# Performance work log

Measured on AMD Instinct MI355X. Metric: run time of the kernel, lower is better.

The kernel has to match this reference:

```python
import jax, jax.numpy as jnp
import numpy as np

N_NODES = 100000


def _gcn_layer(h, W, b, src, dst, norm, n):
    # h: [N, Fin] -> transform then normalized scatter-add aggregation
    h = h @ W                                   # [N, Fout]
    msg = h[src] * norm[:, None]                # [E', Fout] gather + scale
    out = jax.ops.segment_sum(msg, dst, num_segments=n)  # scatter-add
    return out + b


def setup_inputs() -> dict:
    key = jax.random.key(0)
    k1, k2, k3, k4 = jax.random.split(key, 4)
    N, F_IN, HID, C, E = N_NODES, 512, 128, 40, 1600000
    x = jax.random.normal(k1, (N, F_IN), dtype=jnp.float32)
    edge_index = jax.random.randint(k2, (2, E), 0, N, dtype=jnp.int64)
    W1 = jax.random.normal(k3, (F_IN, HID), dtype=jnp.float32) * (1.0 / np.sqrt(F_IN))
    b1 = jnp.zeros((HID,), dtype=jnp.float32)
    W2 = jax.random.normal(k4, (HID, C), dtype=jnp.float32) * (1.0 / np.sqrt(HID))
    b2 = jnp.zeros((C,), dtype=jnp.float32)
    return {"x": x, "edge_index": edge_index, "W1": W1, "b1": b1, "W2": W2, "b2": b2}


def reference(x, edge_index, W1, b1, W2, b2):
    n = x.shape[0]
    # add self-loops (GCNConv default)
    loop = jnp.arange(n, dtype=edge_index.dtype)
    src = jnp.concatenate([edge_index[0], loop])
    dst = jnp.concatenate([edge_index[1], loop])
    # symmetric normalization: deg counted on destination (in-degree, incl. self-loop)
    deg = jax.ops.segment_sum(jnp.ones_like(dst, dtype=x.dtype), dst, num_segments=n)
    dis = jnp.where(deg > 0, jax.lax.rsqrt(deg), 0.0)  # deg^{-1/2}
    norm = dis[src] * dis[dst]                          # per-edge weight

    h = jax.nn.relu(_gcn_layer(x, W1, b1, src, dst, norm, n))
    # dropout: identity in eval mode (training=False)
    h = _gcn_layer(h, W2, b2, src, dst, norm, n)
    return jax.nn.log_softmax(h, axis=1)
```

## Files before the change

### kernel.cpp

```cpp
#include <hip/hip_runtime.h>
#include <hip/hip_bf16.h>


#define F_IN 512
#define HID  128
#define NC   40

typedef __attribute__((ext_vector_type(8))) short bf16x8;
typedef __attribute__((ext_vector_type(4))) float f32x4v;

__device__ __forceinline__ ushort f2bf(float f) {
    union { float f; unsigned u; } x; x.f = f;
    unsigned r = x.u + 0x7FFFu + ((x.u >> 16) & 1u);
    return (ushort)(r >> 16);
}
__device__ __forceinline__ float bf2f(ushort u) {
    return __uint_as_float((unsigned)u << 16);
}
__device__ __forceinline__ bf16x8 cvt8(float4 lo, float4 hi) {
    __align__(16) ushort t[8];
    t[0]=f2bf(lo.x); t[1]=f2bf(lo.y); t[2]=f2bf(lo.z); t[3]=f2bf(lo.w);
    t[4]=f2bf(hi.x); t[5]=f2bf(hi.y); t[6]=f2bf(hi.z); t[7]=f2bf(hi.w);
    return *(const bf16x8*)t;
}

__global__ void prep_k(const int* __restrict__ dst, int E, int EB,
                       unsigned* __restrict__ cnt,
                       const float* __restrict__ W1, const float* __restrict__ W2,
                       ushort* __restrict__ W1p, ushort* __restrict__ W2p) {
    int b = blockIdx.x;
    if (b < EB) {
        int t = b * 256 + threadIdx.x;
        if (t < E) atomicAdd(&cnt[dst[t]], 1u);
        return;
    }
    int t = (b - EB) * 256 + threadIdx.x;
    if (t < 65536) {
        int j = t & 7, n = (t >> 3) & 127, kb = (t >> 10) & 3, s = t >> 12;
        int k = s * 32 + kb * 8 + j;
        W1p[t] = f2bf(W1[(size_t)k * HID + n]);
    } else {
        int q = t - 65536;
        if (q < 6144) {
            int j = q & 7;
            int i2 = q >> 3;
            int n = i2 % 48;
            int i3 = i2 / 48;
            int kb = i3 & 3, ks = i3 >> 2;
            int k = ks * 32 + kb * 8 + j;
            float v = (n < NC) ? W2[(size_t)k * NC + n] : 0.f;
            W2p[q] = f2bf(v);
        }
    }
}

__global__ __launch_bounds__(1024) void scan_block(const unsigned* __restrict__ cnt,
                                                   unsigned* __restrict__ offs,
                                                   unsigned* __restrict__ bsums,
                                                   float* __restrict__ dis, int N) {
    int tid = threadIdx.x;
    int i = blockIdx.x * 1024 + tid;
    unsigned v = (i < N) ? cnt[i] : 0u;
    if (i < N) dis[i] = rsqrtf((float)v + 1.0f);
    int lane = tid & 63, w = tid >> 6;
    unsigned s = v;
    #pragma unroll
    for (int d = 1; d < 64; d <<= 1) {
        unsigned t = __shfl_up(s, d, 64);
        if (lane >= d) s += t;
    }
    __shared__ unsigned wt[16];
    if (lane == 63) wt[w] = s;
    __syncthreads();
    unsigned add = 0;
    #pragma unroll
    for (int j = 0; j < 16; j++) add += (j < w) ? wt[j] : 0u;
    unsigned incl = s + add;
    if (i < N) offs[i] = incl - v;
    if (tid == 1023) bsums[blockIdx.x] = incl;
}

__global__ __launch_bounds__(1024) void scan_add2(unsigned* __restrict__ offs,
                                                  const unsigned* __restrict__ bsums,
                                                  int N, unsigned total) {
    int i = blockIdx.x * 1024 + threadIdx.x;
    int lane = threadIdx.x & 63;
    unsigned s = 0;
    for (int j = lane; j < (int)blockIdx.x; j += 64) s += bsums[j];
    #pragma unroll
    for (int d = 1; d < 64; d <<= 1) s += __shfl_xor(s, d, 64);
    if (i < N) offs[i] += s;
    if (i == 0) offs[N] = total;
}

__global__ void fill_csr(const int* __restrict__ src, const int* __restrict__ dst,
                         const unsigned* __restrict__ offs, unsigned* __restrict__ cursor,
                         int* __restrict__ col, int E) {
    int t = blockIdx.x * blockDim.x + threadIdx.x;
    if (t >= E) return;
    int s = src[t], d = dst[t];
    unsigned pos = offs[d] + atomicAdd(&cursor[d], 1u);
    col[pos] = s;
}

__global__ __launch_bounds__(256) void gemm1_mfma(const float* __restrict__ A,
                                                  const ushort* __restrict__ Bp,
                                                  const float* __restrict__ dis,
                                                  ushort* __restrict__ C, int N) {
    const int tid  = threadIdx.x;
    const int wave = tid >> 6;
    const int lane = tid & 63;
    const int quad = lane >> 4;
    const int mr   = lane & 15;
    const int base = (blockIdx.x * 4 + wave) * 32;
    if (base >= N) return;
    const int r0 = base + mr;
    const int r1 = base + 16 + mr;
    const bool ok0 = r0 < N, ok1 = r1 < N;
    const float* ap0 = A + (size_t)(ok0 ? r0 : 0) * F_IN + quad * 8;
    const float* ap1 = A + (size_t)(ok1 ? r1 : 0) * F_IN + quad * 8;
    const ushort* bp = Bp + quad * 1024 + mr * 8;

    f32x4v acc0[8], acc1[8];
    #pragma unroll
    for (int t = 0; t < 8; t++) {
        acc0[t] = (f32x4v){0.f, 0.f, 0.f, 0.f};
        acc1[t] = (f32x4v){0.f, 0.f, 0.f, 0.f};
    }

    float4 av[2][4];
    #pragma unroll
    for (int b = 0; b < 2; b++) {
        av[b][0] = *(const float4*)(ap0 + b * 32);
        av[b][1] = *(const float4*)(ap0 + b * 32 + 4);
        av[b][2] = *(const float4*)(ap1 + b * 32);
        av[b][3] = *(const float4*)(ap1 + b * 32 + 4);
    }

    for (int s = 0; s < 16; s++) {
        bf16x8 fa0 = cvt8(av[s & 1][0], av[s & 1][1]);
        bf16x8 fa1 = cvt8(av[s & 1][2], av[s & 1][3]);
        if (s < 14) {
            av[s & 1][0] = *(const float4*)(ap0 + (s + 2) * 32);
            av[s & 1][1] = *(const float4*)(ap0 + (s + 2) * 32 + 4);
            av[s & 1][2] = *(const float4*)(ap1 + (s + 2) * 32);
            av[s & 1][3] = *(const float4*)(ap1 + (s + 2) * 32 + 4);
        }
        const ushort* bs = bp + s * 4096;
        #pragma unroll
        for (int t = 0; t < 8; t++) {
            bf16x8 b = *(const bf16x8*)(bs + t * 128);
            acc0[t] = __builtin_amdgcn_mfma_f32_16x16x32_bf16(fa0, b, acc0[t], 0, 0, 0);
            acc1[t] = __builtin_amdgcn_mfma_f32_16x16x32_bf16(fa1, b, acc1[t], 0, 0, 0);
        }
    }

    #pragma unroll
    for (int rr = 0; rr < 4; rr++) {
        int ra = base + quad * 4 + rr;
        if (ra < N) {
            float ds = dis[ra];
            #pragma unroll
            for (int t = 0; t < 8; t++)
                C[(size_t)ra * HID + t * 16 + mr] = f2bf(acc0[t][rr] * ds);
        }
        int rb = base + 16 + quad * 4 + rr;
        if (rb < N) {
            float ds = dis[rb];
            #pragma unroll
            for (int t = 0; t < 8; t++)
                C[(size_t)rb * HID + t * 16 + mr] = f2bf(acc1[t][rr] * ds);
        }
    }
}

__global__ __launch_bounds__(256) void agg1_k(const ushort* __restrict__ h,
                                              const int* __restrict__ col,
                                              const unsigned* __restrict__ offs,
                                              const float* __restrict__ dis,
                                              const float* __restrict__ b1,
                                              ushort* __restrict__ out, int N) {
    int node = blockIdx.x * 16 + (threadIdx.x >> 4);
    if (node >= N) return;
    int lane = threadIdx.x & 15;
    const ushort* hb = h + (size_t)lane * 8;
    float a[8];
    {
        uint4 v = *(const uint4*)(hb + (size_t)node * HID);
        const ushort* u = (const ushort*)&v;
        #pragma unroll
        for (int j = 0; j < 8; j++) a[j] = bf2f(u[j]);
    }
    unsigned p0 = offs[node], p1 = offs[node + 1];
    unsigned p = p0;
    while (p < p1 && (p & 3u)) {
        int s = col[p++];
        uint4 v = *(const uint4*)(hb + (size_t)s * HID);
        const ushort* u = (const ushort*)&v;
        #pragma unroll
        for (int j = 0; j < 8; j++) a[j] += bf2f(u[j]);
    }
    unsigned rem = p1 - p;
    const int4* cp = (const int4*)(col + p);
    unsigned nb8 = rem >> 3;
    int4 c0, c1;
    if (nb8) { c0 = cp[0]; c1 = cp[1]; }
    for (unsigned b = 0; b < nb8; b++) {
        uint4 v0 = *(const uint4*)(hb + (size_t)c0.x * HID);
        uint4 v1 = *(const uint4*)(hb + (size_t)c0.y * HID);
        uint4 v2 = *(const uint4*)(hb + (size_t)c0.z * HID);
        uint4 v3 = *(const uint4*)(hb + (size_t)c0.w * HID);
        uint4 v4 = *(const uint4*)(hb + (size_t)c1.x * HID);
        uint4 v5 = *(const uint4*)(hb + (size_t)c1.y * HID);
        uint4 v6 = *(const uint4*)(hb + (size_t)c1.z * HID);
        uint4 v7 = *(const uint4*)(hb + (size_t)c1.w * HID);
        if (b + 1 < nb8) { c0 = cp[2 * b + 2]; c1 = cp[2 * b + 3]; }
        const ushort* u0 = (const ushort*)&v0;
        const ushort* u1 = (const ushort*)&v1;
        const ushort* u2 = (const ushort*)&v2;
        const ushort* u3 = (const ushort*)&v3;
        const ushort* u4 = (const ushort*)&v4;
        const ushort* u5 = (const ushort*)&v5;
        const ushort* u6 = (const ushort*)&v6;
        const ushort* u7 = (const ushort*)&v7;
        #pragma unroll
        for (int j = 0; j < 8; j++) {
            float t0 = bf2f(u0[j]) + bf2f(u1[j]);
            float t1 = bf2f(u2[j]) + bf2f(u3[j]);
            float t2 = bf2f(u4[j]) + bf2f(u5[j]);
            float t3 = bf2f(u6[j]) + bf2f(u7[j]);
            a[j] += (t0 + t1) + (t2 + t3);
        }
    }
    p += nb8 << 3;
    if (rem & 4u) {
        int4 c = *(const int4*)(col + p);
        uint4 v0 = *(const uint4*)(hb + (size_t)c.x * HID);
        uint4 v1 = *(const uint4*)(hb + (size_t)c.y * HID);
        uint4 v2 = *(const uint4*)(hb + (size_t)c.z * HID);
        uint4 v3 = *(const uint4*)(hb + (size_t)c.w * HID);
        const ushort* u0 = (const ushort*)&v0;
        const ushort* u1 = (const ushort*)&v1;
        const ushort* u2 = (const ushort*)&v2;
        const ushort* u3 = (const ushort*)&v3;
        #pragma unroll
        for (int j = 0; j < 8; j++)
            a[j] += (bf2f(u0[j]) + bf2f(u1[j])) + (bf2f(u2[j]) + bf2f(u3[j]));
        p += 4;
    }
    for (; p < p1; ++p) {
        int s = col[p];
        uint4 v = *(const uint4*)(hb + (size_t)s * HID);
        const ushort* u = (const ushort*)&v;
        #pragma unroll
        for (int j = 0; j < 8; j++) a[j] += bf2f(u[j]);
    }
    float dd = dis[node];
    float4 bb0 = *(const float4*)(b1 + lane * 8);
    float4 bb1 = *(const float4*)(b1 + lane * 8 + 4);
    const float bb[8] = {bb0.x, bb0.y, bb0.z, bb0.w, bb1.x, bb1.y, bb1.z, bb1.w};
    __align__(16) ushort o[8];
    #pragma unroll
    for (int j = 0; j < 8; j++) o[j] = f2bf(fmaxf(a[j] * dd + bb[j], 0.f));
    *(uint4*)(out + (size_t)node * HID + (size_t)lane * 8) = *(const uint4*)o;
}

__global__ __launch_bounds__(256) void gemm2_mfma(const ushort* __restrict__ A,
                                                  const ushort* __restrict__ W2p,
                                                  const float* __restrict__ dis,
                                                  ushort* __restrict__ h2, int N) {
    const int tid  = threadIdx.x;
    const int wave = tid >> 6;
    const int lane = tid & 63;
    const int quad = lane >> 4;
    const int mr   = lane & 15;
    const int base = (blockIdx.x * 4 + wave) * 32;
    if (base >= N) return;
    const int r0 = base + mr;
    const int r1 = base + 16 + mr;
    const bool ok0 = r0 < N, ok1 = r1 < N;
    const ushort* ap0 = A + (size_t)(ok0 ? r0 : 0) * HID + quad * 8;
    const ushort* ap1 = A + (size_t)(ok1 ? r1 : 0) * HID + quad * 8;
    const ushort* bp = W2p + quad * 384 + mr * 8;

    f32x4v acc0[3], acc1[3];
    #pragma unroll
    for (int t = 0; t < 3; t++) {
        acc0[t] = (f32x4v){0.f, 0.f, 0.f, 0.f};
        acc1[t] = (f32x4v){0.f, 0.f, 0.f, 0.f};
    }
    #pragma unroll
    for (int ks = 0; ks < 4; ks++) {
        bf16x8 a0 = *(const bf16x8*)(ap0 + ks * 32);
        bf16x8 a1 = *(const bf16x8*)(ap1 + ks * 32);
        #pragma unroll
        for (int t = 0; t < 3; t++) {
            bf16x8 b = *(const bf16x8*)(bp + ks * 1536 + t * 128);
            acc0[t] = __builtin_amdgcn_mfma_f32_16x16x32_bf16(a0, b, acc0[t], 0, 0, 0);
            acc1[t] = __builtin_amdgcn_mfma_f32_16x16x32_bf16(a1, b, acc1[t], 0, 0, 0);
        }
    }
    #pragma unroll
    for (int rr = 0; rr < 4; rr++) {
        int ra = base + quad * 4 + rr;
        if (ra < N) {
            float ds = dis[ra];
            #pragma unroll
            for (int t = 0; t < 3; t++) {
                int c = t * 16 + mr;
                if (c < NC) h2[(size_t)ra * NC + c] = f2bf(acc0[t][rr] * ds);
            }
        }
        int rb = base + 16 + quad * 4 + rr;
        if (rb < N) {
            float ds = dis[rb];
            #pragma unroll
            for (int t = 0; t < 3; t++) {
                int c = t * 16 + mr;
                if (c < NC) h2[(size_t)rb * NC + c] = f2bf(acc1[t][rr] * ds);
            }
        }
    }
}

__global__ __launch_bounds__(256) void agg2_ls(const ushort* __restrict__ h2,
                                               const int* __restrict__ col,
                                               const unsigned* __restrict__ offs,
                                               const float* __restrict__ dis,
                                               const float* __restrict__ b2,
                                               float* __restrict__ out, int N) {
    int node = blockIdx.x * 32 + (threadIdx.x >> 3);
    if (node >= N) return;
    int lane = threadIdx.x & 7;
    const bool act = lane < 5;
    const ushort* hb = h2 + (size_t)lane * 8;
    float a[8] = {};
    if (act) {
        uint4 v = *(const uint4*)(hb + (size_t)node * NC);
        const ushort* u = (const ushort*)&v;
        #pragma unroll
        for (int j = 0; j < 8; j++) a[j] = bf2f(u[j]);
    }
    unsigned p0 = offs[node], p1 = offs[node + 1];
    unsigned p = p0;
    while (p < p1 && (p & 3u)) {
        int s = col[p++];
        if (act) {
            uint4 v = *(const uint4*)(hb + (size_t)s * NC);
            const ushort* u = (const ushort*)&v;
            #pragma unroll
            for (int j = 0; j < 8; j++) a[j] += bf2f(u[j]);
        }
    }
    unsigned rem = p1 - p;
    const int4* cp = (const int4*)(col + p);
    unsigned nb8 = rem >> 3;
    int4 c0, c1;
    if (nb8) { c0 = cp[0]; c1 = cp[1]; }
    for (unsigned b = 0; b < nb8; b++) {
        int s0 = c0.x, s1 = c0.y, s2 = c0.z, s3 = c0.w;
        int s4 = c1.x, s5 = c1.y, s6 = c1.z, s7 = c1.w;
        if (b + 1 < nb8) { c0 = cp[2 * b + 2]; c1 = cp[2 * b + 3]; }
        if (act) {
            uint4 v0 = *(const uint4*)(hb + (size_t)s0 * NC);
            uint4 v1 = *(const uint4*)(hb + (size_t)s1 * NC);
            uint4 v2 = *(const uint4*)(hb + (size_t)s2 * NC);
            uint4 v3 = *(const uint4*)(hb + (size_t)s3 * NC);
            uint4 v4 = *(const uint4*)(hb + (size_t)s4 * NC);
            uint4 v5 = *(const uint4*)(hb + (size_t)s5 * NC);
            uint4 v6 = *(const uint4*)(hb + (size_t)s6 * NC);
            uint4 v7 = *(const uint4*)(hb + (size_t)s7 * NC);
            const ushort* u0 = (const ushort*)&v0;
            const ushort* u1 = (const ushort*)&v1;
            const ushort* u2 = (const ushort*)&v2;
            const ushort* u3 = (const ushort*)&v3;
            const ushort* u4 = (const ushort*)&v4;
            const ushort* u5 = (const ushort*)&v5;
            const ushort* u6 = (const ushort*)&v6;
            const ushort* u7 = (const ushort*)&v7;
            #pragma unroll
            for (int j = 0; j < 8; j++) {
                float t0 = bf2f(u0[j]) + bf2f(u1[j]);
                float t1 = bf2f(u2[j]) + bf2f(u3[j]);
                float t2 = bf2f(u4[j]) + bf2f(u5[j]);
                float t3 = bf2f(u6[j]) + bf2f(u7[j]);
                a[j] += (t0 + t1) + (t2 + t3);
            }
        }
    }
    p += nb8 << 3;
    if (rem & 4u) {
        int4 c = *(const int4*)(col + p);
        if (act) {
            uint4 v0 = *(const uint4*)(hb + (size_t)c.x * NC);
            uint4 v1 = *(const uint4*)(hb + (size_t)c.y * NC);
            uint4 v2 = *(const uint4*)(hb + (size_t)c.z * NC);
            uint4 v3 = *(const uint4*)(hb + (size_t)c.w * NC);
            const ushort* u0 = (const ushort*)&v0;
            const ushort* u1 = (const ushort*)&v1;
            const ushort* u2 = (const ushort*)&v2;
            const ushort* u3 = (const ushort*)&v3;
            #pragma unroll
            for (int j = 0; j < 8; j++)
                a[j] += (bf2f(u0[j]) + bf2f(u1[j])) + (bf2f(u2[j]) + bf2f(u3[j]));
        }
        p += 4;
    }
    for (; p < p1; ++p) {
        int s = col[p];
        if (act) {
            uint4 v = *(const uint4*)(hb + (size_t)s * NC);
            const ushort* u = (const ushort*)&v;
            #pragma unroll
            for (int j = 0; j < 8; j++) a[j] += bf2f(u[j]);
        }
    }
    float dd = dis[node];
    float l[8];
    float m = -1e30f;
    if (act) {
        #pragma unroll
        for (int j = 0; j < 8; j++) {
            l[j] = a[j] * dd + b2[lane * 8 + j];
            m = fmaxf(m, l[j]);
        }
    }
    #pragma unroll
    for (int d = 1; d < 8; d <<= 1) m = fmaxf(m, __shfl_xor(m, d, 8));
    float s = 0.f;
    if (act) {
        #pragma unroll
        for (int j = 0; j < 8; j++) s += __expf(l[j] - m);
    }
    #pragma unroll
    for (int d = 1; d < 8; d <<= 1) s += __shfl_xor(s, d, 8);
    float lse = m + __logf(s);
    if (act) {
        float* op = out + (size_t)node * NC + lane * 8;
        *(float4*)op       = make_float4(l[0]-lse, l[1]-lse, l[2]-lse, l[3]-lse);
        *(float4*)(op + 4) = make_float4(l[4]-lse, l[5]-lse, l[6]-lse, l[7]-lse);
    }
}

extern "C" void kernel_launch(void* const* d_in, const int* in_sizes, int n_in,
                              void* d_out, int out_size, void* d_ws, size_t ws_size,
                              hipStream_t stream) {
    const float* x  = (const float*)d_in[0];
    const int*   ei = (const int*)d_in[1];
    const float* W1 = (const float*)d_in[2];
    const float* b1 = (const float*)d_in[3];
    const float* W2 = (const float*)d_in[4];
    const float* b2 = (const float*)d_in[5];
    float* out = (float*)d_out;

    const int N = in_sizes[0] / F_IN;
    const int E = in_sizes[1] / 2;
    const int* src = ei;
    const int* dst = ei + E;

    char* ws = (char*)d_ws;
    size_t o = 0;
    unsigned* cnt  = (unsigned*)(ws + o); o += (size_t)N * 4;
    unsigned* cur  = (unsigned*)(ws + o); o += (size_t)N * 4;
    float*    dis  = (float*)   (ws + o); o += (size_t)N * 4;
    unsigned* offs = (unsigned*)(ws + o); o += (size_t)(N + 4) * 4;
    unsigned* bsums= (unsigned*)(ws + o); o += 4096;
    int*      col  = (int*)     (ws + o); o += (size_t)E * 4;
    o = (o + 15) & ~(size_t)15;
    ushort*   W1p  = (ushort*)  (ws + o); o += (size_t)F_IN * HID * 2;
    o = (o + 15) & ~(size_t)15;
    ushort*   W2p  = (ushort*)  (ws + o); o += 6144 * 2;
    o = (o + 15) & ~(size_t)15;
    ushort*   h1   = (ushort*)  (ws + o); o += (size_t)N * HID * 2;
    o = (o + 15) & ~(size_t)15;
    ushort*   ag1  = (ushort*)  (ws + o); o += (size_t)N * HID * 2;
    o = (o + 15) & ~(size_t)15;
    ushort*   h2   = (ushort*)  (ws + o); o += (size_t)N * NC * 2;

    const int nb = (N + 1023) / 1024;
    const int EB = (E + 255) / 256;
    const int PB = (65536 + 6144 + 255) / 256;

    hipMemsetAsync(cnt, 0, (size_t)N * 8, stream);
    prep_k<<<EB + PB, 256, 0, stream>>>(dst, E, EB, cnt, W1, W2, W1p, W2p);
    scan_block<<<nb, 1024, 0, stream>>>(cnt, offs, bsums, dis, N);
    scan_add2<<<nb, 1024, 0, stream>>>(offs, bsums, N, (unsigned)E);
    fill_csr<<<(E + 255) / 256, 256, 0, stream>>>(src, dst, offs, cur, col, E);

    gemm1_mfma<<<(N + 127) / 128, 256, 0, stream>>>(x, W1p, dis, h1, N);
    agg1_k<<<(N + 15) / 16, 256, 0, stream>>>(h1, col, offs, dis, b1, ag1, N);

    gemm2_mfma<<<(N + 127) / 128, 256, 0, stream>>>(ag1, W2p, dis, h2, N);
    agg2_ls<<<(N + 31) / 32, 256, 0, stream>>>(h2, col, offs, dis, b2, out, N);
}
```

Before: 597.4 us.

## Fuse CSR fill into GEMM1, widen aggregation to full waves, pad h2, use hardware bf16 pack

Merges the CSR fill kernel and the first GEMM into one launch, with the two kinds of blocks doing independent work. Both aggregation kernels now give each node a full 64-lane wave that splits its neighbour list across sub-groups and combines them with shuffle reductions. This aims to raise memory-level parallelism on the gathers at the cost of idle lanes for low-degree nodes. It also pads the second-layer features to 48 columns so rows are 16-byte aligned, and replaces software bf16 rounding with the v_cvt_pk_bf16_f32 instruction.

```diff
diff --git a/kernel.cpp b/kernel.cpp
--- a/kernel.cpp
+++ b/kernel.cpp
@@ -5,23 +5,29 @@
 #define F_IN 512
 #define HID  128
 #define NC   40
+#define NCP  48
 
 typedef __attribute__((ext_vector_type(8))) short bf16x8;
 typedef __attribute__((ext_vector_type(4))) float f32x4v;
 
 __device__ __forceinline__ ushort f2bf(float f) {
-    union { float f; unsigned u; } x; x.f = f;
-    unsigned r = x.u + 0x7FFFu + ((x.u >> 16) & 1u);
-    return (ushort)(r >> 16);
+    unsigned r;
+    asm("v_cvt_pk_bf16_f32 %0, %1, %1" : "=v"(r) : "v"(f));
+    return (ushort)r;
+}
+__device__ __forceinline__ unsigned cvtpk(float a, float b) {
+    unsigned r;
+    asm("v_cvt_pk_bf16_f32 %0, %1, %2" : "=v"(r) : "v"(a), "v"(b));
+    return r;
 }
 __device__ __forceinline__ float bf2f(ushort u) {
     return __uint_as_float((unsigned)u << 16);
 }
 __device__ __forceinline__ bf16x8 cvt8(float4 lo, float4 hi) {
-    __align__(16) ushort t[8];
-    t[0]=f2bf(lo.x); t[1]=f2bf(lo.y); t[2]=f2bf(lo.z); t[3]=f2bf(lo.w);
-    t[4]=f2bf(hi.x); t[5]=f2bf(hi.y); t[6]=f2bf(hi.z); t[7]=f2bf(hi.w);
-    return *(const bf16x8*)t;
+    union { unsigned u[4]; bf16x8 v; } t;
+    t.u[0] = cvtpk(lo.x, lo.y); t.u[1] = cvtpk(lo.z, lo.w);
+    t.u[2] = cvtpk(hi.x, hi.y); t.u[3] = cvtpk(hi.z, hi.w);
+    return t.v;
 }
 
 __global__ void prep_k(const int* __restrict__ dst, int E, int EB,
@@ -93,20 +99,21 @@
     if (i == 0) offs[N] = total;
 }
 
-__global__ void fill_csr(const int* __restrict__ src, const int* __restrict__ dst,
-                         const unsigned* __restrict__ offs, unsigned* __restrict__ cursor,
-                         int* __restrict__ col, int E) {
-    int t = blockIdx.x * blockDim.x + threadIdx.x;
-    if (t >= E) return;
-    int s = src[t], d = dst[t];
-    unsigned pos = offs[d] + atomicAdd(&cursor[d], 1u);
-    col[pos] = s;
-}
-
-__global__ __launch_bounds__(256) void gemm1_mfma(const float* __restrict__ A,
-                                                  const ushort* __restrict__ Bp,
-                                                  const float* __restrict__ dis,
-                                                  ushort* __restrict__ C, int N) {
+__global__ __launch_bounds__(256) void fill_gemm1(
+        const int* __restrict__ src, const int* __restrict__ dst,
+        const unsigned* __restrict__ offs, unsigned* __restrict__ cursor,
+        int* __restrict__ col, int E, int GB,
+        const float* __restrict__ A, const ushort* __restrict__ Bp,
+        const float* __restrict__ dis, ushort* __restrict__ C, int N) {
+    if (blockIdx.x >= GB) {
+        int t = (blockIdx.x - GB) * 256 + threadIdx.x;
+        if (t < E) {
+            int s = src[t], d = dst[t];
+            unsigned pos = offs[d] + atomicAdd(&cursor[d], 1u);
+            col[pos] = s;
+        }
+        return;
+    }
     const int tid  = threadIdx.x;
     const int wave = tid >> 6;
     const int lane = tid & 63;
@@ -180,89 +187,54 @@
                                               const float* __restrict__ dis,
                                               const float* __restrict__ b1,
                                               ushort* __restrict__ out, int N) {
-    int node = blockIdx.x * 16 + (threadIdx.x >> 4);
+    int node = blockIdx.x * 4 + (threadIdx.x >> 6);
     if (node >= N) return;
-    int lane = threadIdx.x & 15;
-    const ushort* hb = h + (size_t)lane * 8;
-    float a[8];
-    {
+    int lane = threadIdx.x & 63;
+    int ni = lane >> 4;
+    int fl = lane & 15;
+    const ushort* hb = h + (size_t)fl * 8;
+    float a[8] = {0.f, 0.f, 0.f, 0.f, 0.f, 0.f, 0.f, 0.f};
+    if (ni == 0) {
         uint4 v = *(const uint4*)(hb + (size_t)node * HID);
         const ushort* u = (const ushort*)&v;
         #pragma unroll
         for (int j = 0; j < 8; j++) a[j] = bf2f(u[j]);
     }
     unsigned p0 = offs[node], p1 = offs[node + 1];
-    unsigned p = p0;
-    while (p < p1 && (p & 3u)) {
-        int s = col[p++];
-        uint4 v = *(const uint4*)(hb + (size_t)s * HID);
-        const ushort* u = (const ushort*)&v;
-        #pragma unroll
-        for (int j = 0; j < 8; j++) a[j] += bf2f(u[j]);
-    }
-    unsigned rem = p1 - p;
-    const int4* cp = (const int4*)(col + p);
-    unsigned nb8 = rem >> 3;
-    int4 c0, c1;
-    if (nb8) { c0 = cp[0]; c1 = cp[1]; }
-    for (unsigned b = 0; b < nb8; b++) {
-        uint4 v0 = *(const uint4*)(hb + (size_t)c0.x * HID);
-        uint4 v1 = *(const uint4*)(hb + (size_t)c0.y * HID);
-        uint4 v2 = *(const uint4*)(hb + (size_t)c0.z * HID);
-        uint4 v3 = *(const uint4*)(hb + (size_t)c0.w * HID);
-        uint4 v4 = *(const uint4*)(hb + (size_t)c1.x * HID);
-        uint4 v5 = *(const uint4*)(hb + (size_t)c1.y * HID);
-        uint4 v6 = *(const uint4*)(hb + (size_t)c1.z * HID);
-        uint4 v7 = *(const uint4*)(hb + (size_t)c1.w * HID);
-        if (b + 1 < nb8) { c0 = cp[2 * b + 2]; c1 = cp[2 * b + 3]; }
-        const ushort* u0 = (const ushort*)&v0;
-        const ushort* u1 = (const ushort*)&v1;
-        const ushort* u2 = (const ushort*)&v2;
-        const ushort* u3 = (const ushort*)&v3;
-        const ushort* u4 = (const ushort*)&v4;
-        const ushort* u5 = (const ushort*)&v5;
-        const ushort* u6 = (const ushort*)&v6;
-        const ushort* u7 = (const ushort*)&v7;
-        #pragma unroll
-        for (int j = 0; j < 8; j++) {
-            float t0 = bf2f(u0[j]) + bf2f(u1[j]);
-            float t1 = bf2f(u2[j]) + bf2f(u3[j]);
-            float t2 = bf2f(u4[j]) + bf2f(u5[j]);
-            float t3 = bf2f(u6[j]) + bf2f(u7[j]);
-            a[j] += (t0 + t1) + (t2 + t3);
-        }
-    }
-    p += nb8 << 3;
-    if (rem & 4u) {
-        int4 c = *(const int4*)(col + p);
-        uint4 v0 = *(const uint4*)(hb + (size_t)c.x * HID);
-        uint4 v1 = *(const uint4*)(hb + (size_t)c.y * HID);
-        uint4 v2 = *(const uint4*)(hb + (size_t)c.z * HID);
-        uint4 v3 = *(const uint4*)(hb + (size_t)c.w * HID);
-        const ushort* u0 = (const ushort*)&v0;
-        const ushort* u1 = (const ushort*)&v1;
-        const ushort* u2 = (const ushort*)&v2;
-        const ushort* u3 = (const ushort*)&v3;
-        #pragma unroll
-        for (int j = 0; j < 8; j++)
-            a[j] += (bf2f(u0[j]) + bf2f(u1[j])) + (bf2f(u2[j]) + bf2f(u3[j]));
-        p += 4;
-    }
-    for (; p < p1; ++p) {
-        int s = col[p];
-        uint4 v = *(const uint4*)(hb + (size_t)s * HID);
-        const ushort* u = (const ushort*)&v;
-        #pragma unroll
-        for (int j = 0; j < 8; j++) a[j] += bf2f(u[j]);
-    }
-    float dd = dis[node];
-    float4 bb0 = *(const float4*)(b1 + lane * 8);
-    float4 bb1 = *(const float4*)(b1 + lane * 8 + 4);
-    const float bb[8] = {bb0.x, bb0.y, bb0.z, bb0.w, bb1.x, bb1.y, bb1.z, bb1.w};
-    __align__(16) ushort o[8];
-    #pragma unroll
-    for (int j = 0; j < 8; j++) o[j] = f2bf(fmaxf(a[j] * dd + bb[j], 0.f));
-    *(uint4*)(out + (size_t)node * HID + (size_t)lane * 8) = *(const uint4*)o;
+    int sA = (p0 + ni     < p1) ? col[p0 + ni]     : -1;
+    int sB = (p0 + ni + 4 < p1) ? col[p0 + ni + 4] : -1;
+    for (unsigned p = p0; p < p1; p += 8) {
+        int sC = (p + 8 + ni  < p1) ? col[p + 8 + ni]  : -1;
+        int sD = (p + 12 + ni < p1) ? col[p + 12 + ni] : -1;
+        if (sA >= 0) {
+            uint4 v = *(const uint4*)(hb + (size_t)sA * HID);
+            const ushort* u = (const ushort*)&v;
+            #pragma unroll
+            for (int j = 0; j < 8; j++) a[j] += bf2f(u[j]);
+        }
+        if (sB >= 0) {
+            uint4 v = *(const uint4*)(hb + (size_t)sB * HID);
+            const ushort* u = (const ushort*)&v;
+            #pragma unroll
+            for (int j = 0; j < 8; j++) a[j] += bf2f(u[j]);
+        }
+        sA = sC; sB = sD;
+    }
+    #pragma unroll
+    for (int j = 0; j < 8; j++) {
+        a[j] += __shfl_xor(a[j], 16);
+        a[j] += __shfl_xor(a[j], 32);
+    }
+    if (ni == 0) {
+        float dd = dis[node];
+        float4 bb0 = *(const float4*)(b1 + fl * 8);
+        float4 bb1 = *(const float4*)(b1 + fl * 8 + 4);
+        const float bb[8] = {bb0.x, bb0.y, bb0.z, bb0.w, bb1.x, bb1.y, bb1.z, bb1.w};
+        __align__(16) ushort o[8];
+        #pragma unroll
+        for (int j = 0; j < 8; j++) o[j] = f2bf(fmaxf(a[j] * dd + bb[j], 0.f));
+        *(uint4*)(out + (size_t)node * HID + (size_t)fl * 8) = *(const uint4*)o;
+    }
 }
 
 __global__ __launch_bounds__(256) void gemm2_mfma(const ushort* __restrict__ A,
@@ -308,7 +280,7 @@
             #pragma unroll
             for (int t = 0; t < 3; t++) {
                 int c = t * 16 + mr;
-                if (c < NC) h2[(size_t)ra * NC + c] = f2bf(acc0[t][rr] * ds);
+                if (c < NC) h2[(size_t)ra * NCP + c] = f2bf(acc0[t][rr] * ds);
             }
         }
         int rb = base + 16 + quad * 4 + rr;
@@ -317,7 +289,7 @@
             #pragma unroll
             for (int t = 0; t < 3; t++) {
                 int c = t * 16 + mr;
-                if (c < NC) h2[(size_t)rb * NC + c] = f2bf(acc1[t][rr] * ds);
+                if (c < NC) h2[(size_t)rb * NCP + c] = f2bf(acc1[t][rr] * ds);
             }
         }
     }
@@ -329,91 +301,45 @@
                                                const float* __restrict__ dis,
                                                const float* __restrict__ b2,
                                                float* __restrict__ out, int N) {
-    int node = blockIdx.x * 32 + (threadIdx.x >> 3);
+    int node = blockIdx.x * 4 + (threadIdx.x >> 6);
     if (node >= N) return;
-    int lane = threadIdx.x & 7;
-    const bool act = lane < 5;
-    const ushort* hb = h2 + (size_t)lane * 8;
-    float a[8] = {};
-    if (act) {
-        uint4 v = *(const uint4*)(hb + (size_t)node * NC);
+    int lane = threadIdx.x & 63;
+    int ni = lane >> 3;
+    int fl = lane & 7;
+    const bool act = fl < 5;
+    const ushort* hb = h2 + (size_t)fl * 8;
+    float a[8] = {0.f, 0.f, 0.f, 0.f, 0.f, 0.f, 0.f, 0.f};
+    if (ni == 0 && act) {
+        uint4 v = *(const uint4*)(hb + (size_t)node * NCP);
         const ushort* u = (const ushort*)&v;
         #pragma unroll
         for (int j = 0; j < 8; j++) a[j] = bf2f(u[j]);
     }
     unsigned p0 = offs[node], p1 = offs[node + 1];
-    unsigned p = p0;
-    while (p < p1 && (p & 3u)) {
-        int s = col[p++];
-        if (act) {
-            uint4 v = *(const uint4*)(hb + (size_t)s * NC);
+    int sA = (p0 + ni     < p1) ? col[p0 + ni]     : -1;
+    int sB = (p0 + ni + 8 < p1) ? col[p0 + ni + 8] : -1;
+    for (unsigned p = p0; p < p1; p += 16) {
+        int sC = (p + 16 + ni < p1) ? col[p + 16 + ni] : -1;
+        int sD = (p + 24 + ni < p1) ? col[p + 24 + ni] : -1;
+        if (sA >= 0 && act) {
+            uint4 v = *(const uint4*)(hb + (size_t)sA * NCP);
             const ushort* u = (const ushort*)&v;
             #pragma unroll
             for (int j = 0; j < 8; j++) a[j] += bf2f(u[j]);
         }
-    }
-    unsigned rem = p1 - p;
-    const int4* cp = (const int4*)(col + p);
-    unsigned nb8 = rem >> 3;
-    int4 c0, c1;
-    if (nb8) { c0 = cp[0]; c1 = cp[1]; }
-    for (unsigned b = 0; b < nb8; b++) {
-        int s0 = c0.x, s1 = c0.y, s2 = c0.z, s3 = c0.w;
-        int s4 = c1.x, s5 = c1.y, s6 = c1.z, s7 = c1.w;
-        if (b + 1 < nb8) { c0 = cp[2 * b + 2]; c1 = cp[2 * b + 3]; }
-        if (act) {
-            uint4 v0 = *(const uint4*)(hb + (size_t)s0 * NC);
-            uint4 v1 = *(const uint4*)(hb + (size_t)s1 * NC);
-            uint4 v2 = *(const uint4*)(hb + (size_t)s2 * NC);
-            uint4 v3 = *(const uint4*)(hb + (size_t)s3 * NC);
-            uint4 v4 = *(const uint4*)(hb + (size_t)s4 * NC);
-            uint4 v5 = *(const uint4*)(hb + (size_t)s5 * NC);
-            uint4 v6 = *(const uint4*)(hb + (size_t)s6 * NC);
-            uint4 v7 = *(const uint4*)(hb + (size_t)s7 * NC);
-            const ushort* u0 = (const ushort*)&v0;
-            const ushort* u1 = (const ushort*)&v1;
-            const ushort* u2 = (const ushort*)&v2;
-            const ushort* u3 = (const ushort*)&v3;
-            const ushort* u4 = (const ushort*)&v4;
-            const ushort* u5 = (const ushort*)&v5;
-            const ushort* u6 = (const ushort*)&v6;
-            const ushort* u7 = (const ushort*)&v7;
-            #pragma unroll
-            for (int j = 0; j < 8; j++) {
-                float t0 = bf2f(u0[j]) + bf2f(u1[j]);
-                float t1 = bf2f(u2[j]) + bf2f(u3[j]);
-                float t2 = bf2f(u4[j]) + bf2f(u5[j]);
-                float t3 = bf2f(u6[j]) + bf2f(u7[j]);
-                a[j] += (t0 + t1) + (t2 + t3);
-            }
-        }
-    }
-    p += nb8 << 3;
-    if (rem & 4u) {
-        int4 c = *(const int4*)(col + p);
-        if (act) {
-            uint4 v0 = *(const uint4*)(hb + (size_t)c.x * NC);
-            uint4 v1 = *(const uint4*)(hb + (size_t)c.y * NC);
-            uint4 v2 = *(const uint4*)(hb + (size_t)c.z * NC);
-            uint4 v3 = *(const uint4*)(hb + (size_t)c.w * NC);
-            const ushort* u0 = (const ushort*)&v0;
-            const ushort* u1 = (const ushort*)&v1;
-            const ushort* u2 = (const ushort*)&v2;
-            const ushort* u3 = (const ushort*)&v3;
-            #pragma unroll
-            for (int j = 0; j < 8; j++)
-                a[j] += (bf2f(u0[j]) + bf2f(u1[j])) + (bf2f(u2[j]) + bf2f(u3[j]));
-        }
-        p += 4;
-    }
-    for (; p < p1; ++p) {
-        int s = col[p];
-        if (act) {
-            uint4 v = *(const uint4*)(hb + (size_t)s * NC);
+        if (sB >= 0 && act) {
+            uint4 v = *(const uint4*)(hb + (size_t)sB * NCP);
             const ushort* u = (const ushort*)&v;
             #pragma unroll
             for (int j = 0; j < 8; j++) a[j] += bf2f(u[j]);
         }
+        sA = sC; sB = sD;
+    }
+    #pragma unroll
+    for (int j = 0; j < 8; j++) {
+        a[j] += __shfl_xor(a[j], 8);
+        a[j] += __shfl_xor(a[j], 16);
+        a[j] += __shfl_xor(a[j], 32);
     }
     float dd = dis[node];
     float l[8];
@@ -421,7 +347,7 @@
     if (act) {
         #pragma unroll
         for (int j = 0; j < 8; j++) {
-            l[j] = a[j] * dd + b2[lane * 8 + j];
+            l[j] = a[j] * dd + b2[fl * 8 + j];
             m = fmaxf(m, l[j]);
         }
     }
@@ -435,8 +361,8 @@
     #pragma unroll
     for (int d = 1; d < 8; d <<= 1) s += __shfl_xor(s, d, 8);
     float lse = m + __logf(s);
-    if (act) {
-        float* op = out + (size_t)node * NC + lane * 8;
+    if (ni == 0 && act) {
+        float* op = out + (size_t)node * NC + fl * 8;
         *(float4*)op       = make_float4(l[0]-lse, l[1]-lse, l[2]-lse, l[3]-lse);
         *(float4*)(op + 4) = make_float4(l[4]-lse, l[5]-lse, l[6]-lse, l[7]-lse);
     }
@@ -475,21 +401,23 @@
     o = (o + 15) & ~(size_t)15;
     ushort*   ag1  = (ushort*)  (ws + o); o += (size_t)N * HID * 2;
     o = (o + 15) & ~(size_t)15;
-    ushort*   h2   = (ushort*)  (ws + o); o += (size_t)N * NC * 2;
+    ushort*   h2   = (ushort*)  (ws + o); o += (size_t)N * NCP * 2;
 
     const int nb = (N + 1023) / 1024;
     const int EB = (E + 255) / 256;
     const int PB = (65536 + 6144 + 255) / 256;
+    const int GB = (N + 127) / 128;
 
     hipMemsetAsync(cnt, 0, (size_t)N * 8, stream);
     prep_k<<<EB + PB, 256, 0, stream>>>(dst, E, EB, cnt, W1, W2, W1p, W2p);
     scan_block<<<nb, 1024, 0, stream>>>(cnt, offs, bsums, dis, N);
     scan_add2<<<nb, 1024, 0, stream>>>(offs, bsums, N, (unsigned)E);
-    fill_csr<<<(E + 255) / 256, 256, 0, stream>>>(src, dst, offs, cur, col, E);
-
-    gemm1_mfma<<<(N + 127) / 128, 256, 0, stream>>>(x, W1p, dis, h1, N);
-    agg1_k<<<(N + 15) / 16, 256, 0, stream>>>(h1, col, offs, dis, b1, ag1, N);
+
+    fill_gemm1<<<GB + EB, 256, 0, stream>>>(src, dst, offs, cur, col, E, GB,
+                                            x, W1p, dis, h1, N);
+
+    agg1_k<<<(N + 3) / 4, 256, 0, stream>>>(h1, col, offs, dis, b1, ag1, N);
 
     gemm2_mfma<<<(N + 127) / 128, 256, 0, stream>>>(ag1, W2p, dis, h2, N);
-    agg2_ls<<<(N + 31) / 32, 256, 0, stream>>>(h2, col, offs, dis, b2, out, N);
-}
+    agg2_ls<<<(N + 3) / 4, 256, 0, stream>>>(h2, col, offs, dis, b2, out, N);
+}
```

After: 598.8 us. Within noise of the previous version (+0.2%).
